# Optimization experiments

Hardware: AMD Instinct MI355X
Metric: run time of the kernel (lower is better)

## Reference

```python
import jax, jax.numpy as jnp
import numpy as np

H = 512
V = 50000
S = 400
B = 64


def setup_inputs() -> dict:
    key = jax.random.key(0)
    ks = jax.random.split(key, 20)
    inp = {
        'input': jax.random.normal(ks[0], (1, B, H), jnp.float32),
        'encoder_states': jax.random.normal(ks[1], (S, B, H), jnp.float32),
        'oov_enc_mask': jax.random.randint(ks[2], (S, B), 0, 2, jnp.int32),
        'hidden': jnp.zeros((1, B, H), jnp.float32),
        # GRU params (PyTorch layout: gates ordered r, z, n)
        'W_ih': jax.random.normal(ks[3], (3 * H, H), jnp.float32) * 0.02,
        'W_hh': jax.random.normal(ks[4], (3 * H, H), jnp.float32) * 0.02,
        'b_ih': jax.random.normal(ks[5], (3 * H,), jnp.float32) * 0.02,
        'b_hh': jax.random.normal(ks[6], (3 * H,), jnp.float32) * 0.02,
        # output vocab projection Linear(2H, V)
        'out_W': jax.random.normal(ks[7], (V, 2 * H), jnp.float32) * 0.02,
        'out_b': jax.random.normal(ks[8], (V,), jnp.float32) * 0.02,
        # additive attention params
        'v': jax.random.normal(ks[9], (H, 1), jnp.float32) * 0.02,
        'Wh': jax.random.normal(ks[10], (H, H), jnp.float32) * 0.02,
        'Ws': jax.random.normal(ks[11], (H, H), jnp.float32) * 0.02,
        'b_attn': jax.random.normal(ks[12], (1, H), jnp.float32) * 0.02,
        # pointer probability Linears (H -> 1)
        'pWh': jax.random.normal(ks[13], (1, H), jnp.float32) * 0.02,
        'pWs': jax.random.normal(ks[14], (1, H), jnp.float32) * 0.02,
        'pWx': jax.random.normal(ks[15], (1, H), jnp.float32) * 0.02,
        'pWx_b': jax.random.normal(ks[16], (1,), jnp.float32) * 0.02,
    }
    return inp


def reference(input, encoder_states, oov_enc_mask, hidden,
              W_ih, W_hh, b_ih, b_hh, out_W, out_b,
              v, Wh, Ws, b_attn, pWh, pWs, pWx, pWx_b):
    x = input[0]            # (B, H)
    h0 = hidden[0]          # (B, H)

    # --- single-step GRU (PyTorch gate order r, z, n) ---
    gi = x @ W_ih.T + b_ih      # (B, 3H)
    gh = h0 @ W_hh.T + b_hh     # (B, 3H)
    ir, iz, inn = jnp.split(gi, 3, axis=1)
    hr, hz, hn = jnp.split(gh, 3, axis=1)
    r = jax.nn.sigmoid(ir + hr)
    z = jax.nn.sigmoid(iz + hz)
    n = jnp.tanh(inn + r * hn)
    h = (1.0 - z) * n + z * h0          # decoder_state, (B, H)
    hidden_new = h[None]                # (1, B, H)

    # --- Bahdanau additive attention, softmax over seq axis ---
    x1 = jnp.einsum('sbh,hk->sbk', encoder_states, Wh)   # (S, B, H)
    x2 = h @ Ws                                          # (B, H) broadcasts over S
    scores = jnp.squeeze(jnp.tanh(x1 + x2 + b_attn) @ v, 2)  # (S, B)
    attn = jax.nn.softmax(scores, axis=0)                # (S, B)
    attn_bs = attn.T                                     # (B, S)

    context = jnp.einsum('bs,sbh->bh', attn_bs, encoder_states)  # (B, H)
    global_state = jnp.concatenate([h, context], axis=1)         # (B, 2H)

    # --- pointer probability ---
    p = jax.nn.sigmoid(context @ pWh.T + h @ pWs.T + x @ pWx.T + pWx_b)  # (B, 1)

    vocab_distr = p * jax.nn.selu(global_state @ out_W.T + out_b)        # (B, V)
    oov_vocab_distr = (1.0 - p) * (attn_bs * oov_enc_mask.astype(jnp.float32).T)  # (B, S)
    extended_vocab_distr = jnp.concatenate([vocab_distr, oov_vocab_distr], axis=1)

    return extended_vocab_distr, hidden_new, jnp.squeeze(p), attn
```

## Files before the change

kernel.cpp:

```cpp
#include <hip/hip_runtime.h>
#include <cmath>

#define H    512
#define H2   1024
#define V    50000
#define SEQ  400
#define EXT  (V + SEQ)

typedef __attribute__((ext_vector_type(8))) short short8;
typedef __attribute__((ext_vector_type(4))) float floatx4;

__device__ __forceinline__ unsigned short f2bf(float f) {
    unsigned int u = __float_as_uint(f);
    u += 0x7fffu + ((u >> 16) & 1u);
    return (unsigned short)(u >> 16);
}

__device__ __forceinline__ uint4 pack8(float4 a, float4 b) {
    union { unsigned short s[8]; uint4 v; } r;
    r.s[0] = f2bf(a.x); r.s[1] = f2bf(a.y); r.s[2] = f2bf(a.z); r.s[3] = f2bf(a.w);
    r.s[4] = f2bf(b.x); r.s[5] = f2bf(b.y); r.s[6] = f2bf(b.z); r.s[7] = f2bf(b.w);
    return r.v;
}

__global__ __launch_bounds__(256) void k0_transpose(
    const float* __restrict__ Wh, unsigned short* __restrict__ WhT)
{
    __shared__ float T[64][65];
    const int k0 = blockIdx.x * 64, n0 = blockIdx.y * 64;
    const int tid = threadIdx.x;
    #pragma unroll
    for (int i = 0; i < 16; ++i) {
        int e = i * 256 + tid;
        int r = e >> 6, c = e & 63;
        T[r][c] = Wh[(size_t)(k0 + r) * H + n0 + c];
    }
    __syncthreads();
    #pragma unroll
    for (int i = 0; i < 16; ++i) {
        int e = i * 256 + tid;
        int nn = e >> 6, kk = e & 63;
        WhT[(size_t)(n0 + nn) * H + k0 + kk] = f2bf(T[kk][nn]);
    }
}

__global__ __launch_bounds__(256) void k1_gru(
    const float* __restrict__ x, const float* __restrict__ h0,
    const float* __restrict__ W_ih, const float* __restrict__ W_hh,
    const float* __restrict__ b_ih, const float* __restrict__ b_hh,
    float* __restrict__ h_out)
{
    __shared__ float xs[64][68];
    __shared__ float hs[64][68];
    const int tid  = threadIdx.x;
    const int j    = blockIdx.x * 4 + (tid >> 6);
    const int lane = tid & 63;

    float a_ir = 0.f, a_iz = 0.f, a_in = 0.f, a_hr = 0.f, a_hz = 0.f, a_hn = 0.f;
    const float* wr_i = W_ih + (size_t)j * H;
    const float* wz_i = W_ih + (size_t)(H + j) * H;
    const float* wn_i = W_ih + (size_t)(2 * H + j) * H;
    const float* wr_h = W_hh + (size_t)j * H;
    const float* wz_h = W_hh + (size_t)(H + j) * H;
    const float* wn_h = W_hh + (size_t)(2 * H + j) * H;

    for (int kc = 0; kc < H; kc += 64) {
        __syncthreads();
        #pragma unroll
        for (int e = tid; e < 64 * 64; e += 256) {
            int bb = e >> 6, kk = e & 63;
            xs[bb][kk] = x[bb * H + kc + kk];
            hs[bb][kk] = h0[bb * H + kc + kk];
        }
        __syncthreads();
        #pragma unroll
        for (int kk = 0; kk < 64; kk += 4) {
            float4 xv = *(const float4*)&xs[lane][kk];
            float4 hv = *(const float4*)&hs[lane][kk];
            float4 w;
            w = *(const float4*)&wr_i[kc + kk];
            a_ir += w.x * xv.x + w.y * xv.y + w.z * xv.z + w.w * xv.w;
            w = *(const float4*)&wz_i[kc + kk];
            a_iz += w.x * xv.x + w.y * xv.y + w.z * xv.z + w.w * xv.w;
            w = *(const float4*)&wn_i[kc + kk];
            a_in += w.x * xv.x + w.y * xv.y + w.z * xv.z + w.w * xv.w;
            w = *(const float4*)&wr_h[kc + kk];
            a_hr += w.x * hv.x + w.y * hv.y + w.z * hv.z + w.w * hv.w;
            w = *(const float4*)&wz_h[kc + kk];
            a_hz += w.x * hv.x + w.y * hv.y + w.z * hv.z + w.w * hv.w;
            w = *(const float4*)&wn_h[kc + kk];
            a_hn += w.x * hv.x + w.y * hv.y + w.z * hv.z + w.w * hv.w;
        }
    }
    float r = 1.f / (1.f + expf(-(a_ir + b_ih[j] + a_hr + b_hh[j])));
    float z = 1.f / (1.f + expf(-(a_iz + b_ih[H + j] + a_hz + b_hh[H + j])));
    float n = tanhf(a_in + b_ih[2 * H + j] + r * (a_hn + b_hh[2 * H + j]));
    float h0v = h0[lane * H + j];
    h_out[lane * H + j] = (1.f - z) * n + z * h0v;
}

__global__ __launch_bounds__(512) void k2_post(
    const float* __restrict__ h, const float* __restrict__ Ws,
    const float* __restrict__ b_attn, const float* __restrict__ x,
    const float* __restrict__ pWs, const float* __restrict__ pWx,
    const float* __restrict__ pWx_b,
    float* __restrict__ x2, float* __restrict__ pd)
{
    const int b = blockIdx.x;
    const int k = threadIdx.x;
    __shared__ float hsh[H];
    __shared__ float rbuf[8];
    hsh[k] = h[b * H + k];
    __syncthreads();
    float acc = 0.f;
    #pragma unroll 8
    for (int m = 0; m < H; ++m) acc += hsh[m] * Ws[(size_t)m * H + k];
    x2[b * H + k] = acc + b_attn[k];

    float pp = hsh[k] * pWs[k] + x[b * H + k] * pWx[k];
    #pragma unroll
    for (int off = 32; off > 0; off >>= 1) pp += __shfl_down(pp, off, 64);
    if ((k & 63) == 0) rbuf[k >> 6] = pp;
    __syncthreads();
    if (k == 0) {
        float t = pWx_b[0];
        #pragma unroll
        for (int w = 0; w < 8; ++w) t += rbuf[w];
        pd[b] = t;
    }
}

__global__ __launch_bounds__(256) void k3_scores(
    const float* __restrict__ enc, const unsigned short* __restrict__ WhT,
    const float* __restrict__ x2, const float* __restrict__ v,
    float* __restrict__ part)
{
    __shared__ uint4 AsG[512];
    __shared__ uint4 BsG[1024];
    __shared__ float red[4 * 64];
    const int s   = blockIdx.x;
    const int nc  = blockIdx.y;
    const int n0  = nc * 128;
    const int tid  = threadIdx.x;
    const int wave = tid >> 6;
    const int lane = tid & 63;
    const int lrow = lane & 15;
    const int q    = lane >> 4;

    floatx4 acc[4][2];
    #pragma unroll
    for (int mt = 0; mt < 4; ++mt)
        #pragma unroll
        for (int nt = 0; nt < 2; ++nt)
            acc[mt][nt] = (floatx4){0.f, 0.f, 0.f, 0.f};

    const float* Abase = enc + (size_t)s * 64 * H;
    for (int kc = 0; kc < H; kc += 64) {
        __syncthreads();
        #pragma unroll
        for (int c = 0; c < 2; ++c) {
            int idx = c * 256 + tid;
            int m = idx >> 3, j = idx & 7, k8 = j ^ (m & 7);
            const float* src = Abase + m * H + kc + k8 * 8;
            AsG[idx] = pack8(*(const float4*)src, *(const float4*)(src + 4));
        }
        #pragma unroll
        for (int c = 0; c < 4; ++c) {
            int idx = c * 256 + tid;
            int n = idx >> 3, j = idx & 7, k8 = j ^ (n & 7);
            BsG[idx] = *(const uint4*)(WhT + (size_t)(n0 + n) * H + kc + k8 * 8);
        }
        __syncthreads();
        #pragma unroll
        for (int kk8 = 0; kk8 < 8; kk8 += 4) {
            const int k8 = kk8 + q;
            short8 a[4], b[2];
            #pragma unroll
            for (int mt = 0; mt < 4; ++mt) {
                int m = mt * 16 + lrow;
                a[mt] = *(const short8*)&AsG[m * 8 + (k8 ^ (m & 7))];
            }
            #pragma unroll
            for (int nt = 0; nt < 2; ++nt) {
                int n = wave * 32 + nt * 16 + lrow;
                b[nt] = *(const short8*)&BsG[n * 8 + (k8 ^ (n & 7))];
            }
            #pragma unroll
            for (int mt = 0; mt < 4; ++mt)
                #pragma unroll
                for (int nt = 0; nt < 2; ++nt)
                    acc[mt][nt] = __builtin_amdgcn_mfma_f32_16x16x32_bf16(
                        a[mt], b[nt], acc[mt][nt], 0, 0, 0);
        }
    }
    float val[4][4];
    #pragma unroll
    for (int mt = 0; mt < 4; ++mt) {
        #pragma unroll
        for (int r = 0; r < 4; ++r) {
            const int bb = mt * 16 + q * 4 + r;
            float sum = 0.f;
            #pragma unroll
            for (int nt = 0; nt < 2; ++nt) {
                const int n = n0 + wave * 32 + nt * 16 + lrow;
                sum += tanhf(acc[mt][nt][r] + x2[bb * H + n]) * v[n];
            }
            #pragma unroll
            for (int off = 8; off > 0; off >>= 1) sum += __shfl_down(sum, off, 16);
            val[mt][r] = sum;
        }
    }
    if (lrow == 0) {
        #pragma unroll
        for (int mt = 0; mt < 4; ++mt)
            #pragma unroll
            for (int r = 0; r < 4; ++r)
                red[wave * 64 + mt * 16 + q * 4 + r] = val[mt][r];
    }
    __syncthreads();
    if (tid < 64) {
        float sc = red[tid] + red[64 + tid] + red[128 + tid] + red[192 + tid];
        part[((size_t)nc * SEQ + s) * 64 + tid] = sc;
    }
}

__global__ __launch_bounds__(512) void k4_softmax(
    const float* __restrict__ part, float* __restrict__ attn_out)
{
    const int b = blockIdx.x;
    const int t = threadIdx.x;
    __shared__ float red[8];
    __shared__ float smax, ssum;
    float myv = 0.f, val = -1e30f;
    if (t < SEQ) {
        myv = part[((size_t)0 * SEQ + t) * 64 + b]
            + part[((size_t)1 * SEQ + t) * 64 + b]
            + part[((size_t)2 * SEQ + t) * 64 + b]
            + part[((size_t)3 * SEQ + t) * 64 + b];
        val = myv;
    }
    float m = val;
    #pragma unroll
    for (int off = 32; off > 0; off >>= 1) m = fmaxf(m, __shfl_down(m, off, 64));
    if ((t & 63) == 0) red[t >> 6] = m;
    __syncthreads();
    if (t == 0) {
        float mm = red[0];
        #pragma unroll
        for (int w = 1; w < 8; ++w) mm = fmaxf(mm, red[w]);
        smax = mm;
    }
    __syncthreads();
    float e = (t < SEQ) ? expf(myv - smax) : 0.f;
    float ssv = e;
    #pragma unroll
    for (int off = 32; off > 0; off >>= 1) ssv += __shfl_down(ssv, off, 64);
    if ((t & 63) == 0) red[t >> 6] = ssv;
    __syncthreads();
    if (t == 0) {
        float ss = 0.f;
        #pragma unroll
        for (int w = 0; w < 8; ++w) ss += red[w];
        ssum = ss;
    }
    __syncthreads();
    if (t < SEQ) attn_out[t * 64 + b] = e / ssum;
}

__global__ __launch_bounds__(128) void k5_context(
    const float* __restrict__ enc, const float* __restrict__ attn,
    float* __restrict__ ctx)
{
    const int b  = blockIdx.x;
    const int hc = blockIdx.y;
    const int t  = threadIdx.x;
    __shared__ float a_s[SEQ];
    for (int s = t; s < SEQ; s += 128) a_s[s] = attn[s * 64 + b];
    __syncthreads();
    const int hh = hc * 128 + t;
    float acc = 0.f;
    #pragma unroll 4
    for (int s = 0; s < SEQ; ++s)
        acc += a_s[s] * enc[((size_t)s * 64 + b) * H + hh];
    ctx[b * H + hh] = acc;
}

__global__ __launch_bounds__(64) void k5b_p(
    const float* __restrict__ ctx, const float* __restrict__ pWh,
    const float* __restrict__ pd, float* __restrict__ p_out,
    float* __restrict__ p_ws)
{
    const int b = blockIdx.x;
    const int t = threadIdx.x;
    float pp = 0.f;
    #pragma unroll
    for (int k = t; k < H; k += 64) pp += ctx[b * H + k] * pWh[k];
    #pragma unroll
    for (int off = 32; off > 0; off >>= 1) pp += __shfl_down(pp, off, 64);
    if (t == 0) {
        float pv = 1.f / (1.f + expf(-(pp + pd[b])));
        p_out[b] = pv;
        p_ws[b]  = pv;
    }
}

__global__ __launch_bounds__(256) void k6_vocab(
    const float* __restrict__ h, const float* __restrict__ ctx,
    const float* __restrict__ outW, const float* __restrict__ outb,
    const float* __restrict__ p_ws, float* __restrict__ ext)
{
    __shared__ uint4 AsG[512];
    __shared__ uint4 BsG[512];
    __shared__ float p_l[64];
    const int tid  = threadIdx.x;
    const int wave = tid >> 6;
    const int lane = tid & 63;
    const int lrow = lane & 15;
    const int q    = lane >> 4;
    const int v0   = blockIdx.x * 64;

    if (tid < 64) p_l[tid] = p_ws[tid];

    floatx4 acc[4];
    #pragma unroll
    for (int mt = 0; mt < 4; ++mt) acc[mt] = (floatx4){0.f, 0.f, 0.f, 0.f};

    for (int kc = 0; kc < H2; kc += 64) {
        __syncthreads();
        const float* Ab = (kc < H) ? (h + kc) : (ctx + (kc - H));
        #pragma unroll
        for (int c = 0; c < 2; ++c) {
            int idx = c * 256 + tid;
            int m = idx >> 3, j = idx & 7, k8 = j ^ (m & 7);
            const float* src = Ab + m * H + k8 * 8;
            AsG[idx] = pack8(*(const float4*)src, *(const float4*)(src + 4));
        }
        #pragma unroll
        for (int c = 0; c < 2; ++c) {
            int idx = c * 256 + tid;
            int n = idx >> 3, j = idx & 7, k8 = j ^ (n & 7);
            int vr = v0 + n; if (vr >= V) vr = V - 1;
            const float* src = outW + (size_t)vr * H2 + kc + k8 * 8;
            BsG[idx] = pack8(*(const float4*)src, *(const float4*)(src + 4));
        }
        __syncthreads();
        #pragma unroll
        for (int kk8 = 0; kk8 < 8; kk8 += 4) {
            const int k8 = kk8 + q;
            const int n = wave * 16 + lrow;
            short8 b = *(const short8*)&BsG[n * 8 + (k8 ^ (n & 7))];
            #pragma unroll
            for (int mt = 0; mt < 4; ++mt) {
                int m = mt * 16 + lrow;
                short8 a = *(const short8*)&AsG[m * 8 + (k8 ^ (m & 7))];
                acc[mt] = __builtin_amdgcn_mfma_f32_16x16x32_bf16(a, b, acc[mt], 0, 0, 0);
            }
        }
    }
    const int n = v0 + wave * 16 + lrow;
    if (n < V) {
        const float ob = outb[n];
        #pragma unroll
        for (int mt = 0; mt < 4; ++mt) {
            #pragma unroll
            for (int r = 0; r < 4; ++r) {
                const int bb = mt * 16 + q * 4 + r;
                float zz = acc[mt][r] + ob;
                float sv = (zz > 0.f) ? 1.0507009873554805f * zz
                                      : 1.7580993408473766f * (expf(zz) - 1.f);
                ext[(size_t)bb * EXT + n] = p_l[bb] * sv;
            }
        }
    }
}

__global__ __launch_bounds__(256) void k7_oov(
    const float* __restrict__ attn, const int* __restrict__ mask,
    const float* __restrict__ p_ws, float* __restrict__ ext)
{
    int e = blockIdx.x * 256 + threadIdx.x;
    if (e < SEQ * 64) {
        int s = e >> 6, b = e & 63;
        float val = (1.f - p_ws[b]) * attn[e] * (mask[e] ? 1.f : 0.f);
        ext[(size_t)b * EXT + V + s] = val;
    }
}

extern "C" void kernel_launch(void* const* d_in, const int* in_sizes, int n_in,
                              void* d_out, int out_size, void* d_ws, size_t ws_size,
                              hipStream_t stream)
{
    (void)in_sizes; (void)n_in; (void)out_size; (void)ws_size;
    const float* x      = (const float*)d_in[0];
    const float* enc    = (const float*)d_in[1];
    const int*   mask   = (const int*)  d_in[2];
    const float* h0     = (const float*)d_in[3];
    const float* W_ih   = (const float*)d_in[4];
    const float* W_hh   = (const float*)d_in[5];
    const float* b_ih   = (const float*)d_in[6];
    const float* b_hh   = (const float*)d_in[7];
    const float* outW   = (const float*)d_in[8];
    const float* outb   = (const float*)d_in[9];
    const float* v      = (const float*)d_in[10];
    const float* Wh     = (const float*)d_in[11];
    const float* Ws     = (const float*)d_in[12];
    const float* b_attn = (const float*)d_in[13];
    const float* pWh    = (const float*)d_in[14];
    const float* pWs    = (const float*)d_in[15];
    const float* pWx    = (const float*)d_in[16];
    const float* pWx_b  = (const float*)d_in[17];

    float* out        = (float*)d_out;
    float* out_ext    = out;
    float* out_hidden = out + (size_t)64 * EXT;
    float* out_p      = out_hidden + 64 * H;
    float* out_attn   = out_p + 64;

    float* ws      = (float*)d_ws;
    float* ws_x2   = ws;
    float* ws_pd   = ws_x2 + 64 * H;
    float* ws_part = ws_pd + 64;
    float* ws_ctx  = ws_part + 4 * SEQ * 64;
    float* ws_p    = ws_ctx + 64 * H;
    unsigned short* ws_whT = (unsigned short*)(ws_p + 64);

    k0_transpose<<<dim3(8, 8), 256, 0, stream>>>(Wh, ws_whT);
    k1_gru<<<128, 256, 0, stream>>>(x, h0, W_ih, W_hh, b_ih, b_hh, out_hidden);
    k2_post<<<64, 512, 0, stream>>>(out_hidden, Ws, b_attn, x, pWs, pWx, pWx_b,
                                    ws_x2, ws_pd);
    k3_scores<<<dim3(SEQ, 4), 256, 0, stream>>>(enc, ws_whT, ws_x2, v, ws_part);
    k4_softmax<<<64, 512, 0, stream>>>(ws_part, out_attn);
    k5_context<<<dim3(64, 4), 128, 0, stream>>>(enc, out_attn, ws_ctx);
    k5b_p<<<64, 64, 0, stream>>>(ws_ctx, pWh, ws_pd, out_p, ws_p);
    k6_vocab<<<(V + 63) / 64, 256, 0, stream>>>(out_hidden, ws_ctx, outW, outb,
                                                ws_p, out_ext);
    k7_oov<<<(SEQ * 64 + 255) / 256, 256, 0, stream>>>(out_attn, mask, ws_p, out_ext);
}
```

Measured before the change: 556.8 us.

## Move GRU and Ws projection to MFMA, double-buffer GEMMs, split context over S

The GRU gate matmuls and the h@Ws projection now run on bf16 MFMA tiles instead of scalar FP32 dot products. Ws gets a bf16 transpose in the same pass as Wh. The scores and vocab GEMMs gain register-prefetched, double-buffered LDS stages with a single barrier per k-step, and bf16 rounding uses a cheaper perm-based pack. The context reduction is split four ways along the sequence, with a combine kernel that also computes the pointer probability. This trades FP32 precision in the GRU and x2 for tensor-core throughput, and k1 and k2 now launch only 8 blocks each.

```diff
diff --git a/kernel.cpp b/kernel.cpp
--- a/kernel.cpp
+++ b/kernel.cpp
@@ -10,37 +10,45 @@
 typedef __attribute__((ext_vector_type(8))) short short8;
 typedef __attribute__((ext_vector_type(4))) float floatx4;
 
-__device__ __forceinline__ unsigned short f2bf(float f) {
-    unsigned int u = __float_as_uint(f);
-    u += 0x7fffu + ((u >> 16) & 1u);
-    return (unsigned short)(u >> 16);
-}
-
+#define LDS_BARRIER() asm volatile("s_waitcnt lgkmcnt(0)\n\ts_barrier" ::: "memory")
+
+__device__ __forceinline__ unsigned int bfpack2(float lo, float hi) {
+    unsigned int a = __float_as_uint(lo) + 0x8000u;
+    unsigned int b = __float_as_uint(hi) + 0x8000u;
+    return __builtin_amdgcn_perm(b, a, 0x07060302);
+}
 __device__ __forceinline__ uint4 pack8(float4 a, float4 b) {
-    union { unsigned short s[8]; uint4 v; } r;
-    r.s[0] = f2bf(a.x); r.s[1] = f2bf(a.y); r.s[2] = f2bf(a.z); r.s[3] = f2bf(a.w);
-    r.s[4] = f2bf(b.x); r.s[5] = f2bf(b.y); r.s[6] = f2bf(b.z); r.s[7] = f2bf(b.w);
-    return r.v;
-}
+    uint4 r;
+    r.x = bfpack2(a.x, a.y);
+    r.y = bfpack2(a.z, a.w);
+    r.z = bfpack2(b.x, b.y);
+    r.w = bfpack2(b.z, b.w);
+    return r;
+}
+__device__ __forceinline__ float4 ld4(const float* p) { return *(const float4*)p; }
 
 __global__ __launch_bounds__(256) void k0_transpose(
-    const float* __restrict__ Wh, unsigned short* __restrict__ WhT)
+    const float* __restrict__ Wh, const float* __restrict__ Ws,
+    unsigned short* __restrict__ WhT, unsigned short* __restrict__ WsT)
 {
     __shared__ float T[64][65];
+    const float* src = blockIdx.z ? Ws : Wh;
+    unsigned short* dst = blockIdx.z ? WsT : WhT;
     const int k0 = blockIdx.x * 64, n0 = blockIdx.y * 64;
     const int tid = threadIdx.x;
     #pragma unroll
     for (int i = 0; i < 16; ++i) {
         int e = i * 256 + tid;
         int r = e >> 6, c = e & 63;
-        T[r][c] = Wh[(size_t)(k0 + r) * H + n0 + c];
+        T[r][c] = src[(size_t)(k0 + r) * H + n0 + c];
     }
     __syncthreads();
     #pragma unroll
     for (int i = 0; i < 16; ++i) {
         int e = i * 256 + tid;
         int nn = e >> 6, kk = e & 63;
-        WhT[(size_t)(n0 + nn) * H + k0 + kk] = f2bf(T[kk][nn]);
+        unsigned int u = __float_as_uint(T[kk][nn]) + 0x8000u;
+        dst[(size_t)(n0 + nn) * H + k0 + kk] = (unsigned short)(u >> 16);
     }
 }
 
@@ -50,84 +58,132 @@
     const float* __restrict__ b_ih, const float* __restrict__ b_hh,
     float* __restrict__ h_out)
 {
-    __shared__ float xs[64][68];
-    __shared__ float hs[64][68];
+    __shared__ uint4 Ax[512];
+    __shared__ uint4 Ah[512];
+    __shared__ uint4 Bg[6][512];
     const int tid  = threadIdx.x;
-    const int j    = blockIdx.x * 4 + (tid >> 6);
-    const int lane = tid & 63;
-
-    float a_ir = 0.f, a_iz = 0.f, a_in = 0.f, a_hr = 0.f, a_hz = 0.f, a_hn = 0.f;
-    const float* wr_i = W_ih + (size_t)j * H;
-    const float* wz_i = W_ih + (size_t)(H + j) * H;
-    const float* wn_i = W_ih + (size_t)(2 * H + j) * H;
-    const float* wr_h = W_hh + (size_t)j * H;
-    const float* wz_h = W_hh + (size_t)(H + j) * H;
-    const float* wn_h = W_hh + (size_t)(2 * H + j) * H;
+    const int wave = tid >> 6, lane = tid & 63;
+    const int lrow = lane & 15, q = lane >> 4;
+    const int J0   = blockIdx.x * 64;
+
+    floatx4 acc[6][4];
+    #pragma unroll
+    for (int g = 0; g < 6; ++g)
+        #pragma unroll
+        for (int mt = 0; mt < 4; ++mt) acc[g][mt] = (floatx4){0.f, 0.f, 0.f, 0.f};
 
     for (int kc = 0; kc < H; kc += 64) {
         __syncthreads();
         #pragma unroll
-        for (int e = tid; e < 64 * 64; e += 256) {
-            int bb = e >> 6, kk = e & 63;
-            xs[bb][kk] = x[bb * H + kc + kk];
-            hs[bb][kk] = h0[bb * H + kc + kk];
+        for (int c = 0; c < 2; ++c) {
+            int idx = c * 256 + tid;
+            int m = idx >> 3, j2 = idx & 7, k8 = j2 ^ (m & 7);
+            const float* sx = x  + m * H + kc + k8 * 8;
+            const float* sh = h0 + m * H + kc + k8 * 8;
+            Ax[idx] = pack8(ld4(sx), ld4(sx + 4));
+            Ah[idx] = pack8(ld4(sh), ld4(sh + 4));
+        }
+        #pragma unroll
+        for (int g = 0; g < 6; ++g) {
+            const float* Wb = (g < 3) ? W_ih : W_hh;
+            const int go = (g % 3) * H;
+            #pragma unroll
+            for (int c = 0; c < 2; ++c) {
+                int idx = c * 256 + tid;
+                int n = idx >> 3, j2 = idx & 7, k8 = j2 ^ (n & 7);
+                const float* sw = Wb + (size_t)(go + J0 + n) * H + kc + k8 * 8;
+                Bg[g][idx] = pack8(ld4(sw), ld4(sw + 4));
+            }
         }
         __syncthreads();
         #pragma unroll
-        for (int kk = 0; kk < 64; kk += 4) {
-            float4 xv = *(const float4*)&xs[lane][kk];
-            float4 hv = *(const float4*)&hs[lane][kk];
-            float4 w;
-            w = *(const float4*)&wr_i[kc + kk];
-            a_ir += w.x * xv.x + w.y * xv.y + w.z * xv.z + w.w * xv.w;
-            w = *(const float4*)&wz_i[kc + kk];
-            a_iz += w.x * xv.x + w.y * xv.y + w.z * xv.z + w.w * xv.w;
-            w = *(const float4*)&wn_i[kc + kk];
-            a_in += w.x * xv.x + w.y * xv.y + w.z * xv.z + w.w * xv.w;
-            w = *(const float4*)&wr_h[kc + kk];
-            a_hr += w.x * hv.x + w.y * hv.y + w.z * hv.z + w.w * hv.w;
-            w = *(const float4*)&wz_h[kc + kk];
-            a_hz += w.x * hv.x + w.y * hv.y + w.z * hv.z + w.w * hv.w;
-            w = *(const float4*)&wn_h[kc + kk];
-            a_hn += w.x * hv.x + w.y * hv.y + w.z * hv.z + w.w * hv.w;
-        }
-    }
-    float r = 1.f / (1.f + expf(-(a_ir + b_ih[j] + a_hr + b_hh[j])));
-    float z = 1.f / (1.f + expf(-(a_iz + b_ih[H + j] + a_hz + b_hh[H + j])));
-    float n = tanhf(a_in + b_ih[2 * H + j] + r * (a_hn + b_hh[2 * H + j]));
-    float h0v = h0[lane * H + j];
-    h_out[lane * H + j] = (1.f - z) * n + z * h0v;
-}
-
-__global__ __launch_bounds__(512) void k2_post(
-    const float* __restrict__ h, const float* __restrict__ Ws,
-    const float* __restrict__ b_attn, const float* __restrict__ x,
-    const float* __restrict__ pWs, const float* __restrict__ pWx,
-    const float* __restrict__ pWx_b,
-    float* __restrict__ x2, float* __restrict__ pd)
-{
-    const int b = blockIdx.x;
-    const int k = threadIdx.x;
-    __shared__ float hsh[H];
-    __shared__ float rbuf[8];
-    hsh[k] = h[b * H + k];
-    __syncthreads();
-    float acc = 0.f;
-    #pragma unroll 8
-    for (int m = 0; m < H; ++m) acc += hsh[m] * Ws[(size_t)m * H + k];
-    x2[b * H + k] = acc + b_attn[k];
-
-    float pp = hsh[k] * pWs[k] + x[b * H + k] * pWx[k];
-    #pragma unroll
-    for (int off = 32; off > 0; off >>= 1) pp += __shfl_down(pp, off, 64);
-    if ((k & 63) == 0) rbuf[k >> 6] = pp;
-    __syncthreads();
-    if (k == 0) {
-        float t = pWx_b[0];
-        #pragma unroll
-        for (int w = 0; w < 8; ++w) t += rbuf[w];
-        pd[b] = t;
-    }
+        for (int kk8 = 0; kk8 < 8; kk8 += 4) {
+            const int k8 = kk8 + q;
+            short8 ax[4], ah[4];
+            #pragma unroll
+            for (int mt = 0; mt < 4; ++mt) {
+                int m = mt * 16 + lrow;
+                ax[mt] = *(const short8*)&Ax[m * 8 + (k8 ^ (m & 7))];
+                ah[mt] = *(const short8*)&Ah[m * 8 + (k8 ^ (m & 7))];
+            }
+            const int n = wave * 16 + lrow;
+            const int gidx = n * 8 + (k8 ^ (n & 7));
+            #pragma unroll
+            for (int g = 0; g < 6; ++g) {
+                short8 bb = *(const short8*)&Bg[g][gidx];
+                #pragma unroll
+                for (int mt = 0; mt < 4; ++mt)
+                    acc[g][mt] = __builtin_amdgcn_mfma_f32_16x16x32_bf16(
+                        (g < 3) ? ax[mt] : ah[mt], bb, acc[g][mt], 0, 0, 0);
+            }
+        }
+    }
+    const int j = J0 + wave * 16 + lrow;
+    const float bir = b_ih[j], biz = b_ih[H + j], bin = b_ih[2 * H + j];
+    const float bhr = b_hh[j], bhz = b_hh[H + j], bhn = b_hh[2 * H + j];
+    #pragma unroll
+    for (int mt = 0; mt < 4; ++mt) {
+        #pragma unroll
+        for (int r = 0; r < 4; ++r) {
+            const int bb = mt * 16 + q * 4 + r;
+            float rg = 1.f / (1.f + expf(-(acc[0][mt][r] + bir + acc[3][mt][r] + bhr)));
+            float zg = 1.f / (1.f + expf(-(acc[1][mt][r] + biz + acc[4][mt][r] + bhz)));
+            float ng = tanhf(acc[2][mt][r] + bin + rg * (acc[5][mt][r] + bhn));
+            float h0v = h0[bb * H + j];
+            h_out[bb * H + j] = (1.f - zg) * ng + zg * h0v;
+        }
+    }
+}
+
+__global__ __launch_bounds__(256) void k2_x2(
+    const float* __restrict__ h, const unsigned short* __restrict__ WsT,
+    const float* __restrict__ b_attn, float* __restrict__ x2)
+{
+    __shared__ uint4 Ag[512];
+    __shared__ uint4 Bgg[512];
+    const int tid  = threadIdx.x;
+    const int wave = tid >> 6, lane = tid & 63;
+    const int lrow = lane & 15, q = lane >> 4;
+    const int n0   = blockIdx.x * 64;
+
+    floatx4 acc[4];
+    #pragma unroll
+    for (int mt = 0; mt < 4; ++mt) acc[mt] = (floatx4){0.f, 0.f, 0.f, 0.f};
+
+    for (int kc = 0; kc < H; kc += 64) {
+        __syncthreads();
+        #pragma unroll
+        for (int c = 0; c < 2; ++c) {
+            int idx = c * 256 + tid;
+            int m = idx >> 3, j2 = idx & 7, k8 = j2 ^ (m & 7);
+            const float* sh = h + m * H + kc + k8 * 8;
+            Ag[idx] = pack8(ld4(sh), ld4(sh + 4));
+            int n = m, k8b = j2 ^ (n & 7);
+            Bgg[idx] = *(const uint4*)(WsT + (size_t)(n0 + n) * H + kc + k8b * 8);
+        }
+        __syncthreads();
+        #pragma unroll
+        for (int kk8 = 0; kk8 < 8; kk8 += 4) {
+            const int k8 = kk8 + q;
+            const int n = wave * 16 + lrow;
+            short8 bb = *(const short8*)&Bgg[n * 8 + (k8 ^ (n & 7))];
+            #pragma unroll
+            for (int mt = 0; mt < 4; ++mt) {
+                int m = mt * 16 + lrow;
+                short8 a = *(const short8*)&Ag[m * 8 + (k8 ^ (m & 7))];
+                acc[mt] = __builtin_amdgcn_mfma_f32_16x16x32_bf16(a, bb, acc[mt], 0, 0, 0);
+            }
+        }
+    }
+    const int n = n0 + wave * 16 + lrow;
+    const float ba = b_attn[n];
+    #pragma unroll
+    for (int mt = 0; mt < 4; ++mt)
+        #pragma unroll
+        for (int r = 0; r < 4; ++r) {
+            const int bb = mt * 16 + q * 4 + r;
+            x2[bb * H + n] = acc[mt][r] + ba;
+        }
 }
 
 __global__ __launch_bounds__(256) void k3_scores(
@@ -135,42 +191,65 @@
     const float* __restrict__ x2, const float* __restrict__ v,
     float* __restrict__ part)
 {
-    __shared__ uint4 AsG[512];
-    __shared__ uint4 BsG[1024];
-    __shared__ float red[4 * 64];
+    __shared__ uint4 AsG[2][512];
+    __shared__ uint4 BsG[2][1024];
+    __shared__ float red[256];
     const int s   = blockIdx.x;
     const int nc  = blockIdx.y;
     const int n0  = nc * 128;
     const int tid  = threadIdx.x;
-    const int wave = tid >> 6;
-    const int lane = tid & 63;
-    const int lrow = lane & 15;
-    const int q    = lane >> 4;
+    const int wave = tid >> 6, lane = tid & 63;
+    const int lrow = lane & 15, q = lane >> 4;
+
+    const float* Abase = enc + (size_t)s * 64 * H;
+
+    float4 arA[2][2];
+    uint4  arB[4];
+    #pragma unroll
+    for (int c = 0; c < 2; ++c) {
+        int idx = c * 256 + tid;
+        int m = idx >> 3, k8 = (idx & 7) ^ (m & 7);
+        const float* sa = Abase + m * H + k8 * 8;
+        arA[c][0] = ld4(sa); arA[c][1] = ld4(sa + 4);
+    }
+    #pragma unroll
+    for (int c = 0; c < 4; ++c) {
+        int idx = c * 256 + tid;
+        int n = idx >> 3, k8 = (idx & 7) ^ (n & 7);
+        arB[c] = *(const uint4*)(WhT + (size_t)(n0 + n) * H + k8 * 8);
+    }
 
     floatx4 acc[4][2];
     #pragma unroll
     for (int mt = 0; mt < 4; ++mt)
         #pragma unroll
-        for (int nt = 0; nt < 2; ++nt)
-            acc[mt][nt] = (floatx4){0.f, 0.f, 0.f, 0.f};
-
-    const float* Abase = enc + (size_t)s * 64 * H;
-    for (int kc = 0; kc < H; kc += 64) {
-        __syncthreads();
-        #pragma unroll
-        for (int c = 0; c < 2; ++c) {
-            int idx = c * 256 + tid;
-            int m = idx >> 3, j = idx & 7, k8 = j ^ (m & 7);
-            const float* src = Abase + m * H + kc + k8 * 8;
-            AsG[idx] = pack8(*(const float4*)src, *(const float4*)(src + 4));
-        }
-        #pragma unroll
-        for (int c = 0; c < 4; ++c) {
-            int idx = c * 256 + tid;
-            int n = idx >> 3, j = idx & 7, k8 = j ^ (n & 7);
-            BsG[idx] = *(const uint4*)(WhT + (size_t)(n0 + n) * H + kc + k8 * 8);
-        }
-        __syncthreads();
+        for (int nt = 0; nt < 2; ++nt) acc[mt][nt] = (floatx4){0.f, 0.f, 0.f, 0.f};
+
+    for (int kc = 0; kc < 8; ++kc) {
+        const int buf = kc & 1;
+        #pragma unroll
+        for (int c = 0; c < 2; ++c)
+            AsG[buf][c * 256 + tid] = pack8(arA[c][0], arA[c][1]);
+        #pragma unroll
+        for (int c = 0; c < 4; ++c)
+            BsG[buf][c * 256 + tid] = arB[c];
+        if (kc < 7) {
+            const int ko = (kc + 1) * 64;
+            #pragma unroll
+            for (int c = 0; c < 2; ++c) {
+                int idx = c * 256 + tid;
+                int m = idx >> 3, k8 = (idx & 7) ^ (m & 7);
+                const float* sa = Abase + m * H + ko + k8 * 8;
+                arA[c][0] = ld4(sa); arA[c][1] = ld4(sa + 4);
+            }
+            #pragma unroll
+            for (int c = 0; c < 4; ++c) {
+                int idx = c * 256 + tid;
+                int n = idx >> 3, k8 = (idx & 7) ^ (n & 7);
+                arB[c] = *(const uint4*)(WhT + (size_t)(n0 + n) * H + ko + k8 * 8);
+            }
+        }
+        LDS_BARRIER();
         #pragma unroll
         for (int kk8 = 0; kk8 < 8; kk8 += 4) {
             const int k8 = kk8 + q;
@@ -178,12 +257,12 @@
             #pragma unroll
             for (int mt = 0; mt < 4; ++mt) {
                 int m = mt * 16 + lrow;
-                a[mt] = *(const short8*)&AsG[m * 8 + (k8 ^ (m & 7))];
+                a[mt] = *(const short8*)&AsG[buf][m * 8 + (k8 ^ (m & 7))];
             }
             #pragma unroll
             for (int nt = 0; nt < 2; ++nt) {
                 int n = wave * 32 + nt * 16 + lrow;
-                b[nt] = *(const short8*)&BsG[n * 8 + (k8 ^ (n & 7))];
+                b[nt] = *(const short8*)&BsG[buf][n * 8 + (k8 ^ (n & 7))];
             }
             #pragma unroll
             for (int mt = 0; mt < 4; ++mt)
@@ -210,6 +289,7 @@
             val[mt][r] = sum;
         }
     }
+    __syncthreads();
     if (lrow == 0) {
         #pragma unroll
         for (int mt = 0; mt < 4; ++mt)
@@ -269,36 +349,52 @@
 
 __global__ __launch_bounds__(128) void k5_context(
     const float* __restrict__ enc, const float* __restrict__ attn,
-    float* __restrict__ ctx)
+    float* __restrict__ ctxp)
 {
     const int b  = blockIdx.x;
     const int hc = blockIdx.y;
+    const int sg = blockIdx.z;
     const int t  = threadIdx.x;
-    __shared__ float a_s[SEQ];
-    for (int s = t; s < SEQ; s += 128) a_s[s] = attn[s * 64 + b];
+    __shared__ float a_s[100];
+    if (t < 100) a_s[t] = attn[(sg * 100 + t) * 64 + b];
     __syncthreads();
     const int hh = hc * 128 + t;
-    float acc = 0.f;
-    #pragma unroll 4
-    for (int s = 0; s < SEQ; ++s)
-        acc += a_s[s] * enc[((size_t)s * 64 + b) * H + hh];
-    ctx[b * H + hh] = acc;
-}
-
-__global__ __launch_bounds__(64) void k5b_p(
-    const float* __restrict__ ctx, const float* __restrict__ pWh,
-    const float* __restrict__ pd, float* __restrict__ p_out,
-    float* __restrict__ p_ws)
+    const float* p = enc + ((size_t)(sg * 100) * 64 + b) * H + hh;
+    float a0 = 0.f, a1 = 0.f;
+    #pragma unroll 5
+    for (int i = 0; i < 100; i += 2) {
+        a0 += a_s[i]     * p[0];
+        a1 += a_s[i + 1] * p[(size_t)64 * H];
+        p += (size_t)128 * H;
+    }
+    ctxp[((size_t)sg * 64 + b) * H + hh] = a0 + a1;
+}
+
+__global__ __launch_bounds__(512) void k5b_p(
+    const float* __restrict__ ctxp, const float* __restrict__ pWh,
+    const float* __restrict__ hdec, const float* __restrict__ pWs,
+    const float* __restrict__ x, const float* __restrict__ pWx,
+    const float* __restrict__ pWx_b,
+    float* __restrict__ ctx, float* __restrict__ p_out, float* __restrict__ p_ws)
 {
     const int b = blockIdx.x;
     const int t = threadIdx.x;
-    float pp = 0.f;
-    #pragma unroll
-    for (int k = t; k < H; k += 64) pp += ctx[b * H + k] * pWh[k];
-    #pragma unroll
-    for (int off = 32; off > 0; off >>= 1) pp += __shfl_down(pp, off, 64);
+    __shared__ float rbuf[8];
+    float c = ctxp[((size_t)0 * 64 + b) * H + t]
+            + ctxp[((size_t)1 * 64 + b) * H + t]
+            + ctxp[((size_t)2 * 64 + b) * H + t]
+            + ctxp[((size_t)3 * 64 + b) * H + t];
+    ctx[b * H + t] = c;
+    float term = c * pWh[t] + hdec[b * H + t] * pWs[t] + x[b * H + t] * pWx[t];
+    #pragma unroll
+    for (int off = 32; off > 0; off >>= 1) term += __shfl_down(term, off, 64);
+    if ((t & 63) == 0) rbuf[t >> 6] = term;
+    __syncthreads();
     if (t == 0) {
-        float pv = 1.f / (1.f + expf(-(pp + pd[b])));
+        float ssv = pWx_b[0];
+        #pragma unroll
+        for (int w = 0; w < 8; ++w) ssv += rbuf[w];
+        float pv = 1.f / (1.f + expf(-ssv));
         p_out[b] = pv;
         p_ws[b]  = pv;
     }
@@ -309,50 +405,68 @@
     const float* __restrict__ outW, const float* __restrict__ outb,
     const float* __restrict__ p_ws, float* __restrict__ ext)
 {
-    __shared__ uint4 AsG[512];
-    __shared__ uint4 BsG[512];
+    __shared__ uint4 AsG[2][512];
+    __shared__ uint4 BsG[2][512];
     __shared__ float p_l[64];
     const int tid  = threadIdx.x;
-    const int wave = tid >> 6;
-    const int lane = tid & 63;
-    const int lrow = lane & 15;
-    const int q    = lane >> 4;
+    const int wave = tid >> 6, lane = tid & 63;
+    const int lrow = lane & 15, q = lane >> 4;
     const int v0   = blockIdx.x * 64;
 
     if (tid < 64) p_l[tid] = p_ws[tid];
 
-    floatx4 acc[4];
-    #pragma unroll
-    for (int mt = 0; mt < 4; ++mt) acc[mt] = (floatx4){0.f, 0.f, 0.f, 0.f};
-
-    for (int kc = 0; kc < H2; kc += 64) {
-        __syncthreads();
-        const float* Ab = (kc < H) ? (h + kc) : (ctx + (kc - H));
+    float4 arA[2][2], arB[2][2];
+    {
+        const float* Ab = h;
         #pragma unroll
         for (int c = 0; c < 2; ++c) {
             int idx = c * 256 + tid;
-            int m = idx >> 3, j = idx & 7, k8 = j ^ (m & 7);
-            const float* src = Ab + m * H + k8 * 8;
-            AsG[idx] = pack8(*(const float4*)src, *(const float4*)(src + 4));
-        }
+            int m = idx >> 3, k8 = (idx & 7) ^ (m & 7);
+            const float* sa = Ab + m * H + k8 * 8;
+            arA[c][0] = ld4(sa); arA[c][1] = ld4(sa + 4);
+            int n = m, k8b = (idx & 7) ^ (n & 7);
+            int vr = v0 + n; if (vr >= V) vr = V - 1;
+            const float* sb = outW + (size_t)vr * H2 + k8b * 8;
+            arB[c][0] = ld4(sb); arB[c][1] = ld4(sb + 4);
+        }
+    }
+
+    floatx4 acc[4];
+    #pragma unroll
+    for (int mt = 0; mt < 4; ++mt) acc[mt] = (floatx4){0.f, 0.f, 0.f, 0.f};
+
+    for (int kc = 0; kc < 16; ++kc) {
+        const int buf = kc & 1;
         #pragma unroll
         for (int c = 0; c < 2; ++c) {
-            int idx = c * 256 + tid;
-            int n = idx >> 3, j = idx & 7, k8 = j ^ (n & 7);
-            int vr = v0 + n; if (vr >= V) vr = V - 1;
-            const float* src = outW + (size_t)vr * H2 + kc + k8 * 8;
-            BsG[idx] = pack8(*(const float4*)src, *(const float4*)(src + 4));
-        }
-        __syncthreads();
+            AsG[buf][c * 256 + tid] = pack8(arA[c][0], arA[c][1]);
+            BsG[buf][c * 256 + tid] = pack8(arB[c][0], arB[c][1]);
+        }
+        if (kc < 15) {
+            const int ko = (kc + 1) * 64;
+            const float* Ab = (ko < H) ? (h + ko) : (ctx + (ko - H));
+            #pragma unroll
+            for (int c = 0; c < 2; ++c) {
+                int idx = c * 256 + tid;
+                int m = idx >> 3, k8 = (idx & 7) ^ (m & 7);
+                const float* sa = Ab + m * H + k8 * 8;
+                arA[c][0] = ld4(sa); arA[c][1] = ld4(sa + 4);
+                int n = m, k8b = (idx & 7) ^ (n & 7);
+                int vr = v0 + n; if (vr >= V) vr = V - 1;
+                const float* sb = outW + (size_t)vr * H2 + ko + k8b * 8;
+                arB[c][0] = ld4(sb); arB[c][1] = ld4(sb + 4);
+            }
+        }
+        LDS_BARRIER();
         #pragma unroll
         for (int kk8 = 0; kk8 < 8; kk8 += 4) {
             const int k8 = kk8 + q;
             const int n = wave * 16 + lrow;
-            short8 b = *(const short8*)&BsG[n * 8 + (k8 ^ (n & 7))];
+            short8 b = *(const short8*)&BsG[buf][n * 8 + (k8 ^ (n & 7))];
             #pragma unroll
             for (int mt = 0; mt < 4; ++mt) {
                 int m = mt * 16 + lrow;
-                short8 a = *(const short8*)&AsG[m * 8 + (k8 ^ (m & 7))];
+                short8 a = *(const short8*)&AsG[buf][m * 8 + (k8 ^ (m & 7))];
                 acc[mt] = __builtin_amdgcn_mfma_f32_16x16x32_bf16(a, b, acc[mt], 0, 0, 0);
             }
         }
@@ -416,22 +530,23 @@
     float* out_p      = out_hidden + 64 * H;
     float* out_attn   = out_p + 64;
 
-    float* ws      = (float*)d_ws;
-    float* ws_x2   = ws;
-    float* ws_pd   = ws_x2 + 64 * H;
-    float* ws_part = ws_pd + 64;
-    float* ws_ctx  = ws_part + 4 * SEQ * 64;
-    float* ws_p    = ws_ctx + 64 * H;
+    float* ws       = (float*)d_ws;
+    float* ws_x2    = ws;
+    float* ws_part  = ws_x2 + 64 * H;
+    float* ws_ctxp  = ws_part + 4 * SEQ * 64;
+    float* ws_ctx   = ws_ctxp + 4 * 64 * H;
+    float* ws_p     = ws_ctx + 64 * H;
     unsigned short* ws_whT = (unsigned short*)(ws_p + 64);
-
-    k0_transpose<<<dim3(8, 8), 256, 0, stream>>>(Wh, ws_whT);
-    k1_gru<<<128, 256, 0, stream>>>(x, h0, W_ih, W_hh, b_ih, b_hh, out_hidden);
-    k2_post<<<64, 512, 0, stream>>>(out_hidden, Ws, b_attn, x, pWs, pWx, pWx_b,
-                                    ws_x2, ws_pd);
+    unsigned short* ws_wsT = ws_whT + (size_t)H * H;
+
+    k0_transpose<<<dim3(8, 8, 2), 256, 0, stream>>>(Wh, Ws, ws_whT, ws_wsT);
+    k1_gru<<<8, 256, 0, stream>>>(x, h0, W_ih, W_hh, b_ih, b_hh, out_hidden);
+    k2_x2<<<8, 256, 0, stream>>>(out_hidden, ws_wsT, b_attn, ws_x2);
     k3_scores<<<dim3(SEQ, 4), 256, 0, stream>>>(enc, ws_whT, ws_x2, v, ws_part);
     k4_softmax<<<64, 512, 0, stream>>>(ws_part, out_attn);
-    k5_context<<<dim3(64, 4), 128, 0, stream>>>(enc, out_attn, ws_ctx);
-    k5b_p<<<64, 64, 0, stream>>>(ws_ctx, pWh, ws_pd, out_p, ws_p);
+    k5_context<<<dim3(64, 4, 4), 128, 0, stream>>>(enc, out_attn, ws_ctxp);
+    k5b_p<<<64, 512, 0, stream>>>(ws_ctxp, pWh, out_hidden, pWs, x, pWx, pWx_b,
+                                  ws_ctx, out_p, ws_p);
     k6_vocab<<<(V + 63) / 64, 256, 0, stream>>>(out_hidden, ws_ctx, outW, outb,
                                                 ws_p, out_ext);
     k7_oov<<<(SEQ * 64 + 255) / 256, 256, 0, stream>>>(out_attn, mask, ws_p, out_ext);
```

New measurement: 520.0 us. 6.6% less time.
